# Optimization experiments

Measured on AMD Instinct MI355X. Metric: run time of the kernel, lower is better.

The kernel has to match this reference:

```python
import jax, jax.numpy as jnp
import numpy as np

B, T, I, H, OUT, L = 256, 1200, 16, 128, 1, 2


def _lstm_layer(x, W_ih, W_hh, b_ih, b_hh):
    # x: [B, T, Din]; W_ih: [4H, Din]; W_hh: [4H, H]
    # Precompute input contribution for all timesteps (one big GEMM),
    # then scan only the recurrent part.
    pre = jnp.einsum('btd,gd->btg', x, W_ih) + b_ih + b_hh  # [B, T, 4H]
    pre = jnp.swapaxes(pre, 0, 1)  # [T, B, 4H]
    h0 = jnp.zeros((x.shape[0], W_hh.shape[1]), dtype=x.dtype)
    c0 = jnp.zeros_like(h0)

    def step(carry, p_t):
        h, c = carry
        g = p_t + h @ W_hh.T  # [B, 4H]
        i, f, gg, o = jnp.split(g, 4, axis=-1)  # torch gate order: i, f, g, o
        i = jax.nn.sigmoid(i)
        f = jax.nn.sigmoid(f)
        gg = jnp.tanh(gg)
        o = jax.nn.sigmoid(o)
        c = f * c + i * gg
        h = o * jnp.tanh(c)
        return (h, c), h

    (_, _), hs = jax.lax.scan(step, (h0, c0), pre)  # hs: [T, B, H]
    return jnp.swapaxes(hs, 0, 1)  # [B, T, H]


def setup_inputs() -> dict:
    key = jax.random.key(0)
    ks = jax.random.split(key, 12)
    s = 0.08  # small init scale to keep gates unsaturated
    inp = {
        'x': jax.random.normal(ks[0], (B, T, I), dtype=jnp.float32),
        'W_ih0': jax.random.normal(ks[1], (4 * H, I), dtype=jnp.float32) * s,
        'W_hh0': jax.random.normal(ks[2], (4 * H, H), dtype=jnp.float32) * s,
        'b_ih0': jax.random.normal(ks[3], (4 * H,), dtype=jnp.float32) * s,
        'b_hh0': jax.random.normal(ks[4], (4 * H,), dtype=jnp.float32) * s,
        'W_ih1': jax.random.normal(ks[5], (4 * H, H), dtype=jnp.float32) * s,
        'W_hh1': jax.random.normal(ks[6], (4 * H, H), dtype=jnp.float32) * s,
        'b_ih1': jax.random.normal(ks[7], (4 * H,), dtype=jnp.float32) * s,
        'b_hh1': jax.random.normal(ks[8], (4 * H,), dtype=jnp.float32) * s,
        'W_lin': jax.random.normal(ks[9], (OUT, H), dtype=jnp.float32) * s,
        'b_lin': jax.random.normal(ks[10], (OUT,), dtype=jnp.float32) * s,
    }
    return inp


def reference(x, W_ih0, W_hh0, b_ih0, b_hh0, W_ih1, W_hh1, b_ih1, b_hh1, W_lin, b_lin):
    h1 = _lstm_layer(x, W_ih0, W_hh0, b_ih0, b_hh0)   # [B, T, H]
    h2 = _lstm_layer(h1, W_ih1, W_hh1, b_ih1, b_hh1)  # [B, T, H]
    out = jax.nn.relu(h2)
    out = jnp.einsum('bth,oh->bto', out, W_lin) + b_lin  # [B, T, OUT]
    return out.reshape(-1, 12)  # [B*T*OUT/12, 12]
```

## Files before the change

kernel.cpp:

```cpp
#include <hip/hip_runtime.h>
#include <hip/hip_fp16.h>

#define B_ 256
#define T_ 1200
#define I_ 16
#define H_ 128

typedef __attribute__((ext_vector_type(2))) _Float16 h2;
typedef __attribute__((ext_vector_type(8))) _Float16 f16x8;

union f16x8u { f16x8 v; h2 h[4]; };

#if __has_builtin(__builtin_amdgcn_fdot2)
__device__ __forceinline__ float fdot2(h2 a, h2 b, float c) {
  return __builtin_amdgcn_fdot2(a, b, c, false);
}
#else
__device__ __forceinline__ float fdot2(h2 a, h2 b, float c) {
  return fmaf((float)a.x, (float)b.x, fmaf((float)a.y, (float)b.y, c));
}
#endif

__device__ __forceinline__ float qsum(float x) {
  x += __int_as_float(__builtin_amdgcn_update_dpp(0, __float_as_int(x), 0xB1, 0xF, 0xF, true));
  x += __int_as_float(__builtin_amdgcn_update_dpp(0, __float_as_int(x), 0x4E, 0xF, 0xF, true));
  return x;
}

__device__ __forceinline__ float sigm(float x) {
  return __builtin_amdgcn_rcpf(1.f + __expf(-x));
}
__device__ __forceinline__ float tanh_(float x) {
  return 1.f - 2.f * __builtin_amdgcn_rcpf(1.f + __expf(2.f * x));
}

__global__ __launch_bounds__(512, 2) void lstm_fused(
    const float* __restrict__ xin,
    const float* __restrict__ Wih0, const float* __restrict__ Whh0,
    const float* __restrict__ bih0, const float* __restrict__ bhh0,
    const float* __restrict__ Wih1, const float* __restrict__ Whh1,
    const float* __restrict__ bih1, const float* __restrict__ bhh1,
    const float* __restrict__ Wlin, const float* __restrict__ blin,
    float* __restrict__ out)
{
  __shared__ __align__(16) __half buf0[2][H_];
  __shared__ __align__(16) __half buf1[2][H_];
  __shared__ __align__(16) float red[2][8];

  const int tid = threadIdx.x;
  const int c = tid & 3;
  const int j = tid >> 2;
  const int b = blockIdx.x;
  const int wv = tid >> 6;

  h2 w0[4][16], wi[4][16], wh[4][16];
  h2 wx[4][2];
  float bs0[4], bs1[4];

#pragma unroll
  for (int q = 0; q < 4; ++q) {
    const int g = q * H_ + j;
    const float* p0 = Whh0 + (size_t)g * H_ + c * 32;
    const float* p1 = Wih1 + (size_t)g * H_ + c * 32;
    const float* p2 = Whh1 + (size_t)g * H_ + c * 32;
#pragma unroll
    for (int i = 0; i < 8; ++i) {
      float4 v = *(const float4*)(p0 + 4 * i);
      w0[q][2*i].x   = (_Float16)v.x; w0[q][2*i].y   = (_Float16)v.y;
      w0[q][2*i+1].x = (_Float16)v.z; w0[q][2*i+1].y = (_Float16)v.w;
      v = *(const float4*)(p1 + 4 * i);
      wi[q][2*i].x   = (_Float16)v.x; wi[q][2*i].y   = (_Float16)v.y;
      wi[q][2*i+1].x = (_Float16)v.z; wi[q][2*i+1].y = (_Float16)v.w;
      v = *(const float4*)(p2 + 4 * i);
      wh[q][2*i].x   = (_Float16)v.x; wh[q][2*i].y   = (_Float16)v.y;
      wh[q][2*i+1].x = (_Float16)v.z; wh[q][2*i+1].y = (_Float16)v.w;
    }
    const float4 vx = *(const float4*)(Wih0 + (size_t)g * I_ + 4 * c);
    wx[q][0].x = (_Float16)vx.x; wx[q][0].y = (_Float16)vx.y;
    wx[q][1].x = (_Float16)vx.z; wx[q][1].y = (_Float16)vx.w;
    bs0[q] = bih0[g] + bhh0[g];
    bs1[q] = bih1[g] + bhh1[g];
  }
  const float wl4 = Wlin[j] * 0.25f;
  const float bl = blin[0];

  if (tid < H_) {
    buf0[0][tid] = __float2half(0.f);
    buf1[0][tid] = __float2half(0.f);
  }
  float cst0 = 0.f, cst1 = 0.f;
  const float* xp = xin + (size_t)b * T_ * I_ + 4 * c;
  float* op = out + (size_t)b * T_;
  __syncthreads();

#pragma unroll 2
  for (int t = 0; t < T_; ++t) {
    const int rb = t & 1;
    const float4 xv = *(const float4*)xp; xp += I_;
    float a0 = 0.f, a1 = 0.f, a2 = 0.f, a3 = 0.f;
#pragma unroll
    for (int i = 0; i < 4; ++i) {
      f16x8u u; u.v = *(const f16x8*)(&buf0[rb][c * 32 + i * 8]);
#pragma unroll
      for (int p = 0; p < 4; ++p) {
        const h2 hv = u.h[p];
        a0 = fdot2(w0[0][4 * i + p], hv, a0);
        a1 = fdot2(w0[1][4 * i + p], hv, a1);
        a2 = fdot2(w0[2][4 * i + p], hv, a2);
        a3 = fdot2(w0[3][4 * i + p], hv, a3);
      }
    }
    h2 xa, xb;
    xa.x = (_Float16)xv.x; xa.y = (_Float16)xv.y;
    xb.x = (_Float16)xv.z; xb.y = (_Float16)xv.w;
    a0 = fdot2(wx[0][0], xa, fdot2(wx[0][1], xb, a0));
    a1 = fdot2(wx[1][0], xa, fdot2(wx[1][1], xb, a1));
    a2 = fdot2(wx[2][0], xa, fdot2(wx[2][1], xb, a2));
    a3 = fdot2(wx[3][0], xa, fdot2(wx[3][1], xb, a3));
    {
      const float g0 = qsum(a0) + bs0[0];
      const float g1 = qsum(a1) + bs0[1];
      const float g2 = qsum(a2) + bs0[2];
      const float g3 = qsum(a3) + bs0[3];
      const float ig = sigm(g0), fg = sigm(g1), gg = tanh_(g2), og = sigm(g3);
      cst0 = fg * cst0 + ig * gg;
      const float h0v = og * tanh_(cst0);
      if (c == 0) buf0[rb ^ 1][j] = __float2half(h0v);
    }
    __syncthreads();
    a0 = 0.f; a1 = 0.f; a2 = 0.f; a3 = 0.f;
#pragma unroll
    for (int i = 0; i < 4; ++i) {
      f16x8u u; u.v = *(const f16x8*)(&buf0[rb ^ 1][c * 32 + i * 8]);
#pragma unroll
      for (int p = 0; p < 4; ++p) {
        const h2 hv = u.h[p];
        a0 = fdot2(wi[0][4 * i + p], hv, a0);
        a1 = fdot2(wi[1][4 * i + p], hv, a1);
        a2 = fdot2(wi[2][4 * i + p], hv, a2);
        a3 = fdot2(wi[3][4 * i + p], hv, a3);
      }
    }
#pragma unroll
    for (int i = 0; i < 4; ++i) {
      f16x8u u; u.v = *(const f16x8*)(&buf1[rb][c * 32 + i * 8]);
#pragma unroll
      for (int p = 0; p < 4; ++p) {
        const h2 hv = u.h[p];
        a0 = fdot2(wh[0][4 * i + p], hv, a0);
        a1 = fdot2(wh[1][4 * i + p], hv, a1);
        a2 = fdot2(wh[2][4 * i + p], hv, a2);
        a3 = fdot2(wh[3][4 * i + p], hv, a3);
      }
    }
    const float g0 = qsum(a0) + bs1[0];
    const float g1 = qsum(a1) + bs1[1];
    const float g2 = qsum(a2) + bs1[2];
    const float g3 = qsum(a3) + bs1[3];
    const float ig = sigm(g0), fg = sigm(g1), gg = tanh_(g2), og = sigm(g3);
    cst1 = fg * cst1 + ig * gg;
    const float h1v = og * tanh_(cst1);
    if (c == 0) buf1[rb ^ 1][j] = __float2half(h1v);
    float val = fmaxf(h1v, 0.f) * wl4;
    val += __shfl_xor(val, 1);
    val += __shfl_xor(val, 2);
    val += __shfl_xor(val, 4);
    val += __shfl_xor(val, 8);
    val += __shfl_xor(val, 16);
    val += __shfl_xor(val, 32);
    if ((tid & 63) == 0) red[rb][wv] = val;
    __syncthreads();
    if (tid == ((t & 7) << 6)) {
      const float4 r0 = *(const float4*)(&red[rb][0]);
      const float4 r1 = *(const float4*)(&red[rb][4]);
      op[t] = bl + r0.x + r0.y + r0.z + r0.w + r1.x + r1.y + r1.z + r1.w;
    }
  }
}

extern "C" void kernel_launch(void* const* d_in, const int* in_sizes, int n_in,
                              void* d_out, int out_size, void* d_ws, size_t ws_size,
                              hipStream_t stream) {
  lstm_fused<<<B_, 512, 0, stream>>>(
      (const float*)d_in[0],
      (const float*)d_in[1], (const float*)d_in[2],
      (const float*)d_in[3], (const float*)d_in[4],
      (const float*)d_in[5], (const float*)d_in[6],
      (const float*)d_in[7], (const float*)d_in[8],
      (const float*)d_in[9], (const float*)d_in[10],
      (float*)d_out);
}
```

Baseline: 2.029 ms.

## Skew the two LSTM layers into one barrier per step and use 1024 threads

Layer 1 now runs one timestep behind layer 0, so both layers' dot products for a step share a single barrier, where before each step needed two. The block grows to 1024 threads, with 8 lanes per hidden unit instead of 4, which halves the per-thread weight registers and dot-product chain length. Biases are pre-scaled by 1/8 and folded into the accumulators, and the output reduction is deferred by one step. In exchange, the lane reduction needs a cross-lane shuffle, and the larger block may limit occupancy.

Result: slower. 5.767 ms (+184.3%).

```diff
diff --git a/kernel.cpp b/kernel.cpp
--- a/kernel.cpp
+++ b/kernel.cpp
@@ -11,19 +11,14 @@
 
 union f16x8u { f16x8 v; h2 h[4]; };
 
-#if __has_builtin(__builtin_amdgcn_fdot2)
 __device__ __forceinline__ float fdot2(h2 a, h2 b, float c) {
   return __builtin_amdgcn_fdot2(a, b, c, false);
 }
-#else
-__device__ __forceinline__ float fdot2(h2 a, h2 b, float c) {
-  return fmaf((float)a.x, (float)b.x, fmaf((float)a.y, (float)b.y, c));
-}
-#endif
 
-__device__ __forceinline__ float qsum(float x) {
+__device__ __forceinline__ float qsum8(float x) {
   x += __int_as_float(__builtin_amdgcn_update_dpp(0, __float_as_int(x), 0xB1, 0xF, 0xF, true));
   x += __int_as_float(__builtin_amdgcn_update_dpp(0, __float_as_int(x), 0x4E, 0xF, 0xF, true));
+  x += __shfl_xor(x, 4);
   return x;
 }
 
@@ -34,7 +29,7 @@
   return 1.f - 2.f * __builtin_amdgcn_rcpf(1.f + __expf(2.f * x));
 }
 
-__global__ __launch_bounds__(512, 2) void lstm_fused(
+__global__ __launch_bounds__(1024, 4) void lstm_fused(
     const float* __restrict__ xin,
     const float* __restrict__ Wih0, const float* __restrict__ Whh0,
     const float* __restrict__ bih0, const float* __restrict__ bhh0,
@@ -45,26 +40,25 @@
 {
   __shared__ __align__(16) __half buf0[2][H_];
   __shared__ __align__(16) __half buf1[2][H_];
-  __shared__ __align__(16) float red[2][8];
+  __shared__ __align__(16) float red[2][16];
 
   const int tid = threadIdx.x;
-  const int c = tid & 3;
-  const int j = tid >> 2;
+  const int c = tid & 7;
+  const int j = tid >> 3;
   const int b = blockIdx.x;
   const int wv = tid >> 6;
 
-  h2 w0[4][16], wi[4][16], wh[4][16];
-  h2 wx[4][2];
+  h2 w0[4][8], wi[4][8], wh[4][8], wx[4];
   float bs0[4], bs1[4];
 
 #pragma unroll
   for (int q = 0; q < 4; ++q) {
     const int g = q * H_ + j;
-    const float* p0 = Whh0 + (size_t)g * H_ + c * 32;
-    const float* p1 = Wih1 + (size_t)g * H_ + c * 32;
-    const float* p2 = Whh1 + (size_t)g * H_ + c * 32;
+    const float* p0 = Whh0 + g * H_ + c * 16;
+    const float* p1 = Wih1 + g * H_ + c * 16;
+    const float* p2 = Whh1 + g * H_ + c * 16;
 #pragma unroll
-    for (int i = 0; i < 8; ++i) {
+    for (int i = 0; i < 4; ++i) {
       float4 v = *(const float4*)(p0 + 4 * i);
       w0[q][2*i].x   = (_Float16)v.x; w0[q][2*i].y   = (_Float16)v.y;
       w0[q][2*i+1].x = (_Float16)v.z; w0[q][2*i+1].y = (_Float16)v.w;
@@ -75,113 +69,118 @@
       wh[q][2*i].x   = (_Float16)v.x; wh[q][2*i].y   = (_Float16)v.y;
       wh[q][2*i+1].x = (_Float16)v.z; wh[q][2*i+1].y = (_Float16)v.w;
     }
-    const float4 vx = *(const float4*)(Wih0 + (size_t)g * I_ + 4 * c);
-    wx[q][0].x = (_Float16)vx.x; wx[q][0].y = (_Float16)vx.y;
-    wx[q][1].x = (_Float16)vx.z; wx[q][1].y = (_Float16)vx.w;
-    bs0[q] = bih0[g] + bhh0[g];
-    bs1[q] = bih1[g] + bhh1[g];
+    const float2 vx = *(const float2*)(Wih0 + g * I_ + 2 * c);
+    wx[q].x = (_Float16)vx.x; wx[q].y = (_Float16)vx.y;
+    bs0[q] = (bih0[g] + bhh0[g]) * 0.125f;
+    bs1[q] = (bih1[g] + bhh1[g]) * 0.125f;
   }
-  const float wl4 = Wlin[j] * 0.25f;
+  const float wl = Wlin[j];
   const float bl = blin[0];
 
   if (tid < H_) {
-    buf0[0][tid] = __float2half(0.f);
-    buf1[0][tid] = __float2half(0.f);
+    const __half z = __float2half(0.f);
+    buf0[0][tid] = z; buf0[1][tid] = z;
+    buf1[0][tid] = z; buf1[1][tid] = z;
   }
   float cst0 = 0.f, cst1 = 0.f;
-  const float* xp = xin + (size_t)b * T_ * I_ + 4 * c;
-  float* op = out + (size_t)b * T_;
+  const float* xp = xin + b * (T_ * I_) + 2 * c;
   __syncthreads();
 
-#pragma unroll 2
-  for (int t = 0; t < T_; ++t) {
+  for (int t = 0; t <= T_; ++t) {
     const int rb = t & 1;
-    const float4 xv = *(const float4*)xp; xp += I_;
-    float a0 = 0.f, a1 = 0.f, a2 = 0.f, a3 = 0.f;
+
+    if (t >= 2 && tid == (((t - 2) & 15) << 6)) {
+      const float4 r0 = *(const float4*)(&red[rb ^ 1][0]);
+      const float4 r1 = *(const float4*)(&red[rb ^ 1][4]);
+      const float4 r2 = *(const float4*)(&red[rb ^ 1][8]);
+      const float4 r3 = *(const float4*)(&red[rb ^ 1][12]);
+      out[b * T_ + (t - 2)] = bl +
+          r0.x + r0.y + r0.z + r0.w + r1.x + r1.y + r1.z + r1.w +
+          r2.x + r2.y + r2.z + r2.w + r3.x + r3.y + r3.z + r3.w;
+    }
+
+    float2 xv = make_float2(0.f, 0.f);
+    if (t < T_) { xv = *(const float2*)xp; xp += I_; }
+
+    float a0 = bs0[0], a1 = bs0[1], a2 = bs0[2], a3 = bs0[3];
+    float b0 = bs1[0], b1 = bs1[1], b2 = bs1[2], b3 = bs1[3];
+    const __half* h0p = &buf0[rb ^ 1][c * 16];
+    const __half* h1p = &buf1[rb][c * 16];
+
 #pragma unroll
-    for (int i = 0; i < 4; ++i) {
-      f16x8u u; u.v = *(const f16x8*)(&buf0[rb][c * 32 + i * 8]);
+    for (int i = 0; i < 2; ++i) {
+      f16x8u u; u.v = *(const f16x8*)(h0p + 8 * i);
 #pragma unroll
       for (int p = 0; p < 4; ++p) {
         const h2 hv = u.h[p];
-        a0 = fdot2(w0[0][4 * i + p], hv, a0);
-        a1 = fdot2(w0[1][4 * i + p], hv, a1);
-        a2 = fdot2(w0[2][4 * i + p], hv, a2);
-        a3 = fdot2(w0[3][4 * i + p], hv, a3);
+        const int w = 4 * i + p;
+        a0 = fdot2(w0[0][w], hv, a0);
+        a1 = fdot2(w0[1][w], hv, a1);
+        a2 = fdot2(w0[2][w], hv, a2);
+        a3 = fdot2(w0[3][w], hv, a3);
+        b0 = fdot2(wi[0][w], hv, b0);
+        b1 = fdot2(wi[1][w], hv, b1);
+        b2 = fdot2(wi[2][w], hv, b2);
+        b3 = fdot2(wi[3][w], hv, b3);
       }
     }
-    h2 xa, xb;
-    xa.x = (_Float16)xv.x; xa.y = (_Float16)xv.y;
-    xb.x = (_Float16)xv.z; xb.y = (_Float16)xv.w;
-    a0 = fdot2(wx[0][0], xa, fdot2(wx[0][1], xb, a0));
-    a1 = fdot2(wx[1][0], xa, fdot2(wx[1][1], xb, a1));
-    a2 = fdot2(wx[2][0], xa, fdot2(wx[2][1], xb, a2));
-    a3 = fdot2(wx[3][0], xa, fdot2(wx[3][1], xb, a3));
-    {
-      const float g0 = qsum(a0) + bs0[0];
-      const float g1 = qsum(a1) + bs0[1];
-      const float g2 = qsum(a2) + bs0[2];
-      const float g3 = qsum(a3) + bs0[3];
+#pragma unroll
+    for (int i = 0; i < 2; ++i) {
+      f16x8u u; u.v = *(const f16x8*)(h1p + 8 * i);
+#pragma unroll
+      for (int p = 0; p < 4; ++p) {
+        const h2 hv = u.h[p];
+        const int w = 4 * i + p;
+        b0 = fdot2(wh[0][w], hv, b0);
+        b1 = fdot2(wh[1][w], hv, b1);
+        b2 = fdot2(wh[2][w], hv, b2);
+        b3 = fdot2(wh[3][w], hv, b3);
+      }
+    }
+    h2 xa; xa.x = (_Float16)xv.x; xa.y = (_Float16)xv.y;
+    a0 = fdot2(wx[0], xa, a0);
+    a1 = fdot2(wx[1], xa, a1);
+    a2 = fdot2(wx[2], xa, a2);
+    a3 = fdot2(wx[3], xa, a3);
+
+    if (t < T_) {
+      const float g0 = qsum8(a0), g1 = qsum8(a1), g2 = qsum8(a2), g3 = qsum8(a3);
       const float ig = sigm(g0), fg = sigm(g1), gg = tanh_(g2), og = sigm(g3);
       cst0 = fg * cst0 + ig * gg;
       const float h0v = og * tanh_(cst0);
-      if (c == 0) buf0[rb ^ 1][j] = __float2half(h0v);
+      if (c == 0) buf0[rb][j] = __float2half(h0v);
+    }
+    if (t >= 1) {
+      const float g0 = qsum8(b0), g1 = qsum8(b1), g2 = qsum8(b2), g3 = qsum8(b3);
+      const float ig = sigm(g0), fg = sigm(g1), gg = tanh_(g2), og = sigm(g3);
+      cst1 = fg * cst1 + ig * gg;
+      const float h1v = og * tanh_(cst1);
+      if (c == 0) buf1[rb ^ 1][j] = __float2half(h1v);
+      float val = fmaxf(h1v, 0.f) * wl;
+      val += __shfl_xor(val, 8);
+      val += __shfl_xor(val, 16);
+      val += __shfl_xor(val, 32);
+      if ((tid & 63) == 0) red[rb][wv] = val;
     }
     __syncthreads();
-    a0 = 0.f; a1 = 0.f; a2 = 0.f; a3 = 0.f;
-#pragma unroll
-    for (int i = 0; i < 4; ++i) {
-      f16x8u u; u.v = *(const f16x8*)(&buf0[rb ^ 1][c * 32 + i * 8]);
-#pragma unroll
-      for (int p = 0; p < 4; ++p) {
-        const h2 hv = u.h[p];
-        a0 = fdot2(wi[0][4 * i + p], hv, a0);
-        a1 = fdot2(wi[1][4 * i + p], hv, a1);
-        a2 = fdot2(wi[2][4 * i + p], hv, a2);
-        a3 = fdot2(wi[3][4 * i + p], hv, a3);
-      }
-    }
-#pragma unroll
-    for (int i = 0; i < 4; ++i) {
-      f16x8u u; u.v = *(const f16x8*)(&buf1[rb][c * 32 + i * 8]);
-#pragma unroll
-      for (int p = 0; p < 4; ++p) {
-        const h2 hv = u.h[p];
-        a0 = fdot2(wh[0][4 * i + p], hv, a0);
-        a1 = fdot2(wh[1][4 * i + p], hv, a1);
-        a2 = fdot2(wh[2][4 * i + p], hv, a2);
-        a3 = fdot2(wh[3][4 * i + p], hv, a3);
-      }
-    }
-    const float g0 = qsum(a0) + bs1[0];
-    const float g1 = qsum(a1) + bs1[1];
-    const float g2 = qsum(a2) + bs1[2];
-    const float g3 = qsum(a3) + bs1[3];
-    const float ig = sigm(g0), fg = sigm(g1), gg = tanh_(g2), og = sigm(g3);
-    cst1 = fg * cst1 + ig * gg;
-    const float h1v = og * tanh_(cst1);
-    if (c == 0) buf1[rb ^ 1][j] = __float2half(h1v);
-    float val = fmaxf(h1v, 0.f) * wl4;
-    val += __shfl_xor(val, 1);
-    val += __shfl_xor(val, 2);
-    val += __shfl_xor(val, 4);
-    val += __shfl_xor(val, 8);
-    val += __shfl_xor(val, 16);
-    val += __shfl_xor(val, 32);
-    if ((tid & 63) == 0) red[rb][wv] = val;
-    __syncthreads();
-    if (tid == ((t & 7) << 6)) {
-      const float4 r0 = *(const float4*)(&red[rb][0]);
-      const float4 r1 = *(const float4*)(&red[rb][4]);
-      op[t] = bl + r0.x + r0.y + r0.z + r0.w + r1.x + r1.y + r1.z + r1.w;
-    }
+  }
+
+  if (tid == 0) {
+    const int s = T_ & 1;
+    const float4 r0 = *(const float4*)(&red[s][0]);
+    const float4 r1 = *(const float4*)(&red[s][4]);
+    const float4 r2 = *(const float4*)(&red[s][8]);
+    const float4 r3 = *(const float4*)(&red[s][12]);
+    out[b * T_ + (T_ - 1)] = bl +
+        r0.x + r0.y + r0.z + r0.w + r1.x + r1.y + r1.z + r1.w +
+        r2.x + r2.y + r2.z + r2.w + r3.x + r3.y + r3.z + r3.w;
   }
 }
 
 extern "C" void kernel_launch(void* const* d_in, const int* in_sizes, int n_in,
                               void* d_out, int out_size, void* d_ws, size_t ws_size,
                               hipStream_t stream) {
-  lstm_fused<<<B_, 512, 0, stream>>>(
+  lstm_fused<<<B_, 1024, 0, stream>>>(
       (const float*)d_in[0],
       (const float*)d_in[1], (const float*)d_in[2],
       (const float*)d_in[3], (const float*)d_in[4],
```
